# Optimization experiments

Measured on AMD Instinct MI355X. Metric: run time of the kernel, lower is better.

The kernel has to match this reference:

```python
import jax, jax.numpy as jnp
import numpy as np

N_NODES = 100000
N_EDGES = 1600000
D = 128
L = 3
D_OUT = 64


def setup_inputs() -> dict:
    key = jax.random.key(0)
    ks = jax.random.split(key, 6)
    x = jax.random.normal(ks[0], (N_NODES, D), dtype=jnp.float32)
    edge_index = jax.random.randint(ks[1], (2, N_EDGES), 0, N_NODES, dtype=jnp.int64)
    # Kaiming-ish init scale for linear layers
    s = 1.0 / np.sqrt(D)
    W_rel = jax.random.normal(ks[2], (L, D, D), dtype=jnp.float32) * s
    b_rel = jnp.zeros((L, D), dtype=jnp.float32)
    W_root = jax.random.normal(ks[3], (L, D, D), dtype=jnp.float32) * s
    fc_w = jax.random.normal(ks[4], (D_OUT, D), dtype=jnp.float32) * s
    fc_b = jnp.zeros((D_OUT,), dtype=jnp.float32)
    return {"x": x, "edge_index": edge_index, "W_rel": W_rel, "b_rel": b_rel,
            "W_root": W_root, "fc_w": fc_w, "fc_b": fc_b}


def reference(x, edge_index, W_rel, b_rel, W_root, fc_w, fc_b):
    # PyG GraphConv (aggr='add'): x_i' = W_root x_i + W_rel * sum_{j in N(i)} x_j + b
    src, dst = edge_index[0], edge_index[1]
    n = x.shape[0]
    num_layers = W_rel.shape[0]  # static small loop over layers
    for l in range(num_layers):
        agg = jax.ops.segment_sum(x[src], dst, num_segments=n)  # [N, D] scatter-add of gathered neighbor feats
        x = agg @ W_rel[l].T + b_rel[l] + x @ W_root[l].T
    return x @ fc_w.T + fc_b
```

## Files before the change

### kernel.cpp

```cpp
#include <hip/hip_runtime.h>


typedef short bf16x8 __attribute__((ext_vector_type(8)));
typedef float f32x4 __attribute__((ext_vector_type(4)));

#define CAPB 8192

__device__ inline float bf2f(unsigned short u) {
    union { unsigned int i; float f; } v; v.i = ((unsigned int)u) << 16; return v.f;
}
__device__ inline unsigned short f2bf(float f) {
    union { float f; unsigned int i; } v; v.f = f;
    unsigned int r = v.i + 0x7FFFu + ((v.i >> 16) & 1u);
    return (unsigned short)(r >> 16);
}

__global__ __launch_bounds__(256) void stages_kernel(
    const float* __restrict__ Wr0, const float* __restrict__ Wo0,
    const float* __restrict__ Wr1, const float* __restrict__ Wo1,
    const float* __restrict__ Wr2, const float* __restrict__ Wo2,
    const float* __restrict__ fcw, const float* __restrict__ fcb,
    const float* __restrict__ br, unsigned short* __restrict__ Nw,
    float* __restrict__ Bv, int* __restrict__ gcur, int NB) {
    int o = blockIdx.x;
    int t = threadIdx.x;
    __shared__ float c02[128], c12[128], c01[128], c11[128], c21[128];
    __shared__ float redbuf[3][128];

    if (o == 0) {
        for (int q = t; q < NB; q += 256) gcur[q] = 0;
    }

    const float* fo = fcw + (size_t)o * 128;
    int i  = t & 127;
    int hi = t >> 7;

    {
        const float* W = hi ? Wr2 : Wo2;
        float acc = 0.f;
        for (int k = 0; k < 128; k++) acc += W[k * 128 + i] * fo[k];
        (hi ? c12 : c02)[i] = acc;
    }
    __syncthreads();

    if (!hi) {
        float a0 = 0.f, a2 = 0.f;
        for (int k = 0; k < 128; k++) {
            float w1o = Wo1[k * 128 + i], w1r = Wr1[k * 128 + i];
            a0 += w1o * c02[k];
            a2 += w1r * c12[k];
        }
        c01[i] = a0; c21[i] = a2;
    } else {
        float a1 = 0.f;
        for (int k = 0; k < 128; k++)
            a1 += Wr1[k * 128 + i] * c02[k] + Wo1[k * 128 + i] * c12[k];
        c11[i] = a1;
    }
    __syncthreads();

    {
        int p = ((o & 3) << 4) | (o >> 2);
        if (!hi) {
            float a0 = 0.f, a2 = 0.f;
            for (int k = 0; k < 128; k++) {
                float w0 = Wo0[k * 128 + i], wr = Wr0[k * 128 + i];
                a0 += w0 * c01[k];
                a2 += wr * c11[k] + w0 * c21[k];
            }
            Nw[(size_t)p * 512 + 0 * 128 + i] = f2bf(a0);
            Nw[(size_t)p * 512 + 2 * 128 + i] = f2bf(a2);
        } else {
            float a1 = 0.f, a3 = 0.f;
            for (int k = 0; k < 128; k++) {
                float w0 = Wo0[k * 128 + i], wr = Wr0[k * 128 + i];
                a1 += wr * c01[k] + w0 * c11[k];
                a3 += wr * c21[k];
            }
            Nw[(size_t)p * 512 + 1 * 128 + i] = f2bf(a1);
            Nw[(size_t)p * 512 + 3 * 128 + i] = f2bf(a3);
        }
    }

    const float* br0 = br;
    const float* br1 = br + 128;
    const float* br2 = br + 256;
    if (!hi) {
        redbuf[0][i] = br2[i] * fo[i] + br1[i] * c02[i] + br0[i] * c01[i];
        redbuf[1][i] = br1[i] * c12[i] + br0[i] * c11[i];
        redbuf[2][i] = br0[i] * c21[i];
    }
    __syncthreads();
    int w = t >> 6, lane = t & 63;
    if (w < 3) {
        float v = redbuf[w][lane] + redbuf[w][lane + 64];
        for (int off = 32; off; off >>= 1) v += __shfl_down(v, off);
        if (lane == 0) Bv[w * 64 + o] = v + (w == 0 ? fcb[o] : 0.f);
    }
}

__global__ __launch_bounds__(512) void prep_kernel(
    const int* __restrict__ src, const int* __restrict__ dst,
    int* __restrict__ gcur, unsigned int* __restrict__ bucketed, int e, int NA, int NB) {
    int b = blockIdx.x, t = threadIdx.x;
    if (b < NA) {
        __shared__ int sHist[512], sScan[512], sExcl[512], sGbase[512];
        __shared__ unsigned int lbuf[2048];
        __shared__ unsigned short lbkt[2048];
        int e0 = b * 2048;
        int cnt = e - e0; if (cnt > 2048) cnt = 2048;
        sHist[t] = 0;
        __syncthreads();
        unsigned int pk[4]; int bk[4];
#pragma unroll
        for (int k = 0; k < 4; k++) {
            int j = t + k * 512;
            if (j < cnt) {
                int d = dst[e0 + j], s = src[e0 + j];
                bk[k] = d >> 8;
                pk[k] = ((unsigned int)s << 8) | (unsigned int)(d & 255);
                atomicAdd(&sHist[bk[k]], 1);
            } else bk[k] = -1;
        }
        __syncthreads();
        int h = sHist[t];
        if (t < NB && h > 0) sGbase[t] = atomicAdd(&gcur[t], h);
        else sGbase[t] = 0;
        int xv = h; sScan[t] = xv; __syncthreads();
        for (int o = 1; o < 512; o <<= 1) {
            int y = (t >= o) ? sScan[t - o] : 0;
            __syncthreads();
            xv += y; sScan[t] = xv;
            __syncthreads();
        }
        sExcl[t] = xv - h;
        sHist[t] = 0;
        __syncthreads();
#pragma unroll
        for (int k = 0; k < 4; k++) {
            if (bk[k] >= 0) {
                int r = atomicAdd(&sHist[bk[k]], 1);
                int pos = sExcl[bk[k]] + r;
                lbuf[pos] = pk[k];
                lbkt[pos] = (unsigned short)bk[k];
            }
        }
        __syncthreads();
        for (int j = t; j < cnt; j += 512) {
            int b2 = lbkt[j];
            int idx = sGbase[b2] + (j - sExcl[b2]);
            if (idx < CAPB) bucketed[(size_t)b2 * CAPB + idx] = lbuf[j];
        }
    }
}

__global__ __launch_bounds__(256) void partB_kernel(
    const unsigned int* __restrict__ bucketed, const int* __restrict__ gcur,
    int* __restrict__ deg, int* __restrict__ start, int* __restrict__ csr, int n) {
    int b = blockIdx.x, t = threadIdx.x;
    __shared__ int ldeg[256], lscan[256], red[256];
    __shared__ int csr_base_s;
    int cnt = gcur[b]; if (cnt > CAPB) cnt = CAPB;
    int part = 0;
    for (int q = t; q < b; q += 256) { int c = gcur[q]; part += (c > CAPB ? CAPB : c); }
    red[t] = part; __syncthreads();
    for (int o = 128; o > 0; o >>= 1) { if (t < o) red[t] += red[t + o]; __syncthreads(); }
    if (t == 0) csr_base_s = red[0];
    ldeg[t] = 0;
    __syncthreads();
    const unsigned int* bd = bucketed + (size_t)b * CAPB;
    for (int j = t; j < cnt; j += 256) atomicAdd(&ldeg[bd[j] & 255], 1);
    __syncthreads();
    int h = ldeg[t];
    int xv = h; lscan[t] = xv; __syncthreads();
    for (int o = 1; o < 256; o <<= 1) {
        int y = (t >= o) ? lscan[t - o] : 0;
        __syncthreads();
        xv += y; lscan[t] = xv;
        __syncthreads();
    }
    int excl = xv - h;
    int csr_base = csr_base_s;
    int node = b * 256 + t;
    if (node < n) { deg[node] = h; start[node] = csr_base + excl; }
    __syncthreads();
    lscan[t] = excl;
    ldeg[t] = 0;
    __syncthreads();
    for (int j = t; j < cnt; j += 256) {
        unsigned int pkd = bd[j];
        int d = pkd & 255;
        int r = atomicAdd(&ldeg[d], 1);
        csr[csr_base + lscan[d] + r] = (int)(pkd >> 8);
    }
}

__global__ __launch_bounds__(256, 4) void gemm_u_kernel(
    const float* __restrict__ x, const unsigned short* __restrict__ Nw,
    unsigned short* __restrict__ U, int n, int NGB) {
    __shared__ unsigned short Blds[8192];
    int bid   = blockIdx.x;
    int matid = (bid >> 3) & 3;
    int blk   = (bid >> 5) * 8 + (bid & 7);
    if (blk >= NGB) return;
    int tid   = threadIdx.x;

    {
        const uint4* nw4 = (const uint4*)Nw;
        uint4* lds4 = (uint4*)Blds;
        for (int g = tid; g < 1024; g += 256) {
            int slot = g & 63;
            int kq   = g >> 6;
            lds4[g] = nw4[(size_t)slot * 64 + matid * 16 + kq];
        }
    }
    __syncthreads();

    int wave = tid >> 6;
    int lane = tid & 63;
    int m    = lane & 15;
    int quad = lane >> 4;
    size_t n64 = (size_t)n * 64;
    unsigned short* up = U + (size_t)matid * n64;

    const int t0 = blk * 16 + wave * 4;

    float4 v[8];
    {
        int arow = t0 * 16 + m; if (arow >= n) arow = n - 1;
        const float* xr = x + (size_t)arow * 128 + quad * 8;
#pragma unroll
        for (int kk = 0; kk < 4; kk++) {
            v[2 * kk]     = *(const float4*)(xr + kk * 32);
            v[2 * kk + 1] = *(const float4*)(xr + kk * 32 + 4);
        }
    }

#pragma unroll
    for (int it = 0; it < 4; it++) {
        int row0 = (t0 + it) * 16;
        if (row0 >= n) break;

        bf16x8 a[4];
#pragma unroll
        for (int kk = 0; kk < 4; kk++) {
            float4 v0 = v[2 * kk], v1 = v[2 * kk + 1];
            a[kk][0] = (short)f2bf(v0.x); a[kk][1] = (short)f2bf(v0.y);
            a[kk][2] = (short)f2bf(v0.z); a[kk][3] = (short)f2bf(v0.w);
            a[kk][4] = (short)f2bf(v1.x); a[kk][5] = (short)f2bf(v1.y);
            a[kk][6] = (short)f2bf(v1.z); a[kk][7] = (short)f2bf(v1.w);
        }

        if (it < 3) {
            int arow = row0 + 16 + m; if (arow >= n) arow = n - 1;
            const float* xr = x + (size_t)arow * 128 + quad * 8;
#pragma unroll
            for (int kk = 0; kk < 4; kk++) {
                v[2 * kk]     = *(const float4*)(xr + kk * 32);
                v[2 * kk + 1] = *(const float4*)(xr + kk * 32 + 4);
            }
        }

        f32x4 acc[4];
#pragma unroll
        for (int t = 0; t < 4; t++) acc[t] = (f32x4){0.f, 0.f, 0.f, 0.f};
#pragma unroll
        for (int kk = 0; kk < 4; kk++) {
            bf16x8 bq[4];
#pragma unroll
            for (int t = 0; t < 4; t++)
                bq[t] = *(const bf16x8*)(Blds + ((kk * 4 + quad) * 64 + t * 16 + m) * 8);
#pragma unroll
            for (int t = 0; t < 4; t++)
                acc[t] = __builtin_amdgcn_mfma_f32_16x16x32_bf16(a[kk], bq[t], acc[t], 0, 0, 0);
        }

#pragma unroll
        for (int r = 0; r < 4; r++) {
            int orow = row0 + quad * 4 + r;
            if (orow < n) {
                ushort4 o4;
                o4.x = f2bf(acc[0][r]); o4.y = f2bf(acc[1][r]);
                o4.z = f2bf(acc[2][r]); o4.w = f2bf(acc[3][r]);
                *(ushort4*)(up + (size_t)orow * 64 + m * 4) = o4;
            }
        }
    }
}

template <int MODE>
__global__ __launch_bounds__(256) void agg64_kernel(
    const unsigned short* __restrict__ in, const unsigned short* __restrict__ addv,
    const int* __restrict__ csr, const int* __restrict__ start, const int* __restrict__ deg,
    unsigned short* __restrict__ outb, float* __restrict__ outf,
    const float* __restrict__ Bv, int* __restrict__ d2w, const int* __restrict__ d2r, int n) {
    int tid = threadIdx.x;
    int fl  = tid & 7;
    int node = blockIdx.x * 32 + (tid >> 3);
    if (node >= n) return;

    float b0[8], b1[8], b2[8];
    if (MODE == 2) {
#pragma unroll
        for (int j = 0; j < 8; j++) {
            int o = fl * 8 + j;
            b0[j] = Bv[o]; b1[j] = Bv[64 + o]; b2[j] = Bv[128 + o];
        }
    }

    int s0 = start[node];
    int d  = deg[node];

    float acc[8];
#pragma unroll
    for (int j = 0; j < 8; j++) acc[j] = 0.f;
    int dsum = 0;

    int d8 = d & ~7;
    for (int e0 = 0; e0 < d8; e0 += 8) {
        int sv[8];
#pragma unroll
        for (int k = 0; k < 8; k++) sv[k] = csr[s0 + e0 + k];
#pragma unroll
        for (int k = 0; k < 8; k++) {
            bf16x8 v = *(const bf16x8*)(in + (size_t)sv[k] * 64 + fl * 8);
#pragma unroll
            for (int j = 0; j < 8; j++) acc[j] += bf2f((unsigned short)v[j]);
            if (MODE == 0 && fl == 0) dsum += deg[sv[k]];
        }
    }
    for (int i = d8; i < d; i++) {
        int s = csr[s0 + i];
        bf16x8 v = *(const bf16x8*)(in + (size_t)s * 64 + fl * 8);
#pragma unroll
        for (int j = 0; j < 8; j++) acc[j] += bf2f((unsigned short)v[j]);
        if (MODE == 0 && fl == 0) dsum += deg[s];
    }
    if (MODE == 0 && fl == 0) d2w[node] = dsum;

    bf16x8 av = *(const bf16x8*)(addv + (size_t)node * 64 + fl * 8);
    if (MODE < 2) {
        bf16x8 o;
#pragma unroll
        for (int j = 0; j < 8; j++) o[j] = (short)f2bf(acc[j] + bf2f((unsigned short)av[j]));
        *(bf16x8*)(outb + (size_t)node * 64 + fl * 8) = o;
    } else {
        float dg = (float)d;
        float dd = (float)d2r[node];
        float ov[8];
#pragma unroll
        for (int j = 0; j < 8; j++)
            ov[j] = acc[j] + bf2f((unsigned short)av[j]) + b0[j] + dg * b1[j] + dd * b2[j];
        float* op = outf + (size_t)node * 64 + fl * 8;
        *(float4*)(op)     = make_float4(ov[0], ov[1], ov[2], ov[3]);
        *(float4*)(op + 4) = make_float4(ov[4], ov[5], ov[6], ov[7]);
    }
}

extern "C" void kernel_launch(void* const* d_in, const int* in_sizes, int n_in,
                              void* d_out, int out_size, void* d_ws, size_t ws_size,
                              hipStream_t stream) {
    const float* x      = (const float*)d_in[0];
    const int*   ei     = (const int*)d_in[1];
    const float* W_rel  = (const float*)d_in[2];
    const float* b_rel  = (const float*)d_in[3];
    const float* W_root = (const float*)d_in[4];
    const float* fc_w   = (const float*)d_in[5];
    const float* fc_b   = (const float*)d_in[6];

    const int n = in_sizes[0] / 128;
    const int e = in_sizes[1] / 2;
    const int* src = ei;
    const int* dst = ei + e;

    const int NB  = (n + 255) >> 8;
    const int NA  = (e + 2047) / 2048;
    const int NT  = (n + 15) / 16;
    const int NGB = (NT + 15) / 16;
    const int NGBp = (NGB + 7) & ~7;

    char* p = (char*)d_ws;
    auto take = [&](size_t bytes) -> void* {
        void* r = (void*)p;
        p += (bytes + 255) & ~(size_t)255;
        return r;
    };
    unsigned short* U  = (unsigned short*)take((size_t)n * 256 * 2);
    unsigned short* w1 = (unsigned short*)take((size_t)n * 64 * 2);
    unsigned short* w2 = (unsigned short*)take((size_t)n * 64 * 2);
    int* deg    = (int*)take((size_t)n * 4);
    int* start  = (int*)take((size_t)n * 4);
    int* d2     = (int*)take((size_t)n * 4);
    int* csr    = (int*)take((size_t)e * 4);
    unsigned int* bucketed = (unsigned int*)take((size_t)NB * CAPB * 4);
    int* gcur   = (int*)take((size_t)NB * 4);
    unsigned short* Nw = (unsigned short*)take(64 * 512 * 2);
    float* Bv   = (float*)take(192 * 4);

    size_t n64 = (size_t)n * 64;
    unsigned short* u0 = U;
    unsigned short* u1 = U + n64;
    unsigned short* u2 = U + 2 * n64;
    unsigned short* u3 = U + 3 * n64;

    stages_kernel<<<64, 256, 0, stream>>>(
        W_rel, W_root, W_rel + 16384, W_root + 16384,
        W_rel + 2 * 16384, W_root + 2 * 16384,
        fc_w, fc_b, b_rel, Nw, Bv, gcur, NB);
    prep_kernel<<<NA, 512, 0, stream>>>(src, dst, gcur, bucketed, e, NA, NB);
    partB_kernel<<<NB, 256, 0, stream>>>(bucketed, gcur, deg, start, csr, n);

    gemm_u_kernel<<<NGBp * 4, 256, 0, stream>>>(x, Nw, U, n, NGB);

    const int AGB = (n + 31) / 32;
    agg64_kernel<0><<<AGB, 256, 0, stream>>>(
        u3, u2, csr, start, deg, w1, nullptr, nullptr, d2, nullptr, n);
    agg64_kernel<1><<<AGB, 256, 0, stream>>>(
        w1, u1, csr, start, deg, w2, nullptr, nullptr, nullptr, nullptr, n);
    agg64_kernel<2><<<AGB, 256, 0, stream>>>(
        w2, u0, csr, start, deg, nullptr, (float*)d_out, Bv, nullptr, d2, n);
}
```

Measured before the change: 307.6 us.

## Fuse edge bucketing and dense GEMM into one launch via block-range dispatch

Merges the edge-bucketing prep kernel and the x·W GEMM kernel into a single launch whose blocks branch on block index, with shared memory unioned between the two roles. The GEMM does not depend on the bucketing, so the two independent workloads can run concurrently and one launch disappears. The cost is that GEMM blocks now launch with 512 threads and half of them exit after staging the weights, which wastes slots and could lower effective occupancy for the GEMM part.

```diff
diff --git a/kernel.cpp b/kernel.cpp
--- a/kernel.cpp
+++ b/kernel.cpp
@@ -99,17 +99,29 @@
     }
 }
 
-__global__ __launch_bounds__(512) void prep_kernel(
+union FusedSmem {
+    struct {
+        int sHist[512], sScan[512], sExcl[512], sGbase[512];
+        unsigned int lbuf[2048];
+        unsigned short lbkt[2048];
+    } pr;
+    unsigned short Blds[8192];
+};
+
+__global__ __launch_bounds__(512, 4) void fused_kernel(
     const int* __restrict__ src, const int* __restrict__ dst,
-    int* __restrict__ gcur, unsigned int* __restrict__ bucketed, int e, int NA, int NB) {
-    int b = blockIdx.x, t = threadIdx.x;
-    if (b < NA) {
-        __shared__ int sHist[512], sScan[512], sExcl[512], sGbase[512];
-        __shared__ unsigned int lbuf[2048];
-        __shared__ unsigned short lbkt[2048];
+    int* __restrict__ gcur, unsigned int* __restrict__ bucketed, int e, int NA, int NB,
+    const float* __restrict__ x, const unsigned short* __restrict__ Nw,
+    unsigned short* __restrict__ U, int n, int NGB) {
+    __shared__ FusedSmem sm;
+    int bid = blockIdx.x;
+    int t   = threadIdx.x;
+
+    if (bid < NA) {
+        int b = bid;
         int e0 = b * 2048;
         int cnt = e - e0; if (cnt > 2048) cnt = 2048;
-        sHist[t] = 0;
+        sm.pr.sHist[t] = 0;
         __syncthreads();
         unsigned int pk[4]; int bk[4];
 #pragma unroll
@@ -119,37 +131,126 @@
                 int d = dst[e0 + j], s = src[e0 + j];
                 bk[k] = d >> 8;
                 pk[k] = ((unsigned int)s << 8) | (unsigned int)(d & 255);
-                atomicAdd(&sHist[bk[k]], 1);
+                atomicAdd(&sm.pr.sHist[bk[k]], 1);
             } else bk[k] = -1;
         }
         __syncthreads();
-        int h = sHist[t];
-        if (t < NB && h > 0) sGbase[t] = atomicAdd(&gcur[t], h);
-        else sGbase[t] = 0;
-        int xv = h; sScan[t] = xv; __syncthreads();
+        int h = sm.pr.sHist[t];
+        if (t < NB && h > 0) sm.pr.sGbase[t] = atomicAdd(&gcur[t], h);
+        else sm.pr.sGbase[t] = 0;
+        int xv = h; sm.pr.sScan[t] = xv; __syncthreads();
         for (int o = 1; o < 512; o <<= 1) {
-            int y = (t >= o) ? sScan[t - o] : 0;
+            int y = (t >= o) ? sm.pr.sScan[t - o] : 0;
             __syncthreads();
-            xv += y; sScan[t] = xv;
+            xv += y; sm.pr.sScan[t] = xv;
             __syncthreads();
         }
-        sExcl[t] = xv - h;
-        sHist[t] = 0;
+        sm.pr.sExcl[t] = xv - h;
+        sm.pr.sHist[t] = 0;
         __syncthreads();
 #pragma unroll
         for (int k = 0; k < 4; k++) {
             if (bk[k] >= 0) {
-                int r = atomicAdd(&sHist[bk[k]], 1);
-                int pos = sExcl[bk[k]] + r;
-                lbuf[pos] = pk[k];
-                lbkt[pos] = (unsigned short)bk[k];
+                int r = atomicAdd(&sm.pr.sHist[bk[k]], 1);
+                int pos = sm.pr.sExcl[bk[k]] + r;
+                sm.pr.lbuf[pos] = pk[k];
+                sm.pr.lbkt[pos] = (unsigned short)bk[k];
             }
         }
         __syncthreads();
         for (int j = t; j < cnt; j += 512) {
-            int b2 = lbkt[j];
-            int idx = sGbase[b2] + (j - sExcl[b2]);
-            if (idx < CAPB) bucketed[(size_t)b2 * CAPB + idx] = lbuf[j];
+            int b2 = sm.pr.lbkt[j];
+            int idx = sm.pr.sGbase[b2] + (j - sm.pr.sExcl[b2]);
+            if (idx < CAPB) bucketed[(size_t)b2 * CAPB + idx] = sm.pr.lbuf[j];
+        }
+        return;
+    }
+
+    int gbid  = bid - NA;
+    int matid = (gbid >> 3) & 3;
+    int blk   = (gbid >> 5) * 8 + (gbid & 7);
+    if (blk >= NGB) return;
+
+    {
+        const uint4* nw4 = (const uint4*)Nw;
+        uint4* lds4 = (uint4*)sm.Blds;
+        for (int g = t; g < 1024; g += 512) {
+            int slot = g & 63;
+            int kq   = g >> 6;
+            lds4[g] = nw4[(size_t)slot * 64 + matid * 16 + kq];
+        }
+    }
+    __syncthreads();
+    if (t >= 256) return;
+
+    int wave = t >> 6;
+    int lane = t & 63;
+    int m    = lane & 15;
+    int quad = lane >> 4;
+    size_t n64 = (size_t)n * 64;
+    unsigned short* up = U + (size_t)matid * n64;
+
+    const int t0 = blk * 16 + wave * 4;
+
+    float4 v[8];
+    {
+        int arow = t0 * 16 + m; if (arow >= n) arow = n - 1;
+        const float* xr = x + (size_t)arow * 128 + quad * 8;
+#pragma unroll
+        for (int kk = 0; kk < 4; kk++) {
+            v[2 * kk]     = *(const float4*)(xr + kk * 32);
+            v[2 * kk + 1] = *(const float4*)(xr + kk * 32 + 4);
+        }
+    }
+
+#pragma unroll
+    for (int it = 0; it < 4; it++) {
+        int row0 = (t0 + it) * 16;
+        if (row0 >= n) break;
+
+        bf16x8 a[4];
+#pragma unroll
+        for (int kk = 0; kk < 4; kk++) {
+            float4 v0 = v[2 * kk], v1 = v[2 * kk + 1];
+            a[kk][0] = (short)f2bf(v0.x); a[kk][1] = (short)f2bf(v0.y);
+            a[kk][2] = (short)f2bf(v0.z); a[kk][3] = (short)f2bf(v0.w);
+            a[kk][4] = (short)f2bf(v1.x); a[kk][5] = (short)f2bf(v1.y);
+            a[kk][6] = (short)f2bf(v1.z); a[kk][7] = (short)f2bf(v1.w);
+        }
+
+        if (it < 3) {
+            int arow = row0 + 16 + m; if (arow >= n) arow = n - 1;
+            const float* xr = x + (size_t)arow * 128 + quad * 8;
+#pragma unroll
+            for (int kk = 0; kk < 4; kk++) {
+                v[2 * kk]     = *(const float4*)(xr + kk * 32);
+                v[2 * kk + 1] = *(const float4*)(xr + kk * 32 + 4);
+            }
+        }
+
+        f32x4 acc[4];
+#pragma unroll
+        for (int tt = 0; tt < 4; tt++) acc[tt] = (f32x4){0.f, 0.f, 0.f, 0.f};
+#pragma unroll
+        for (int kk = 0; kk < 4; kk++) {
+            bf16x8 bq[4];
+#pragma unroll
+            for (int tt = 0; tt < 4; tt++)
+                bq[tt] = *(const bf16x8*)(sm.Blds + ((kk * 4 + quad) * 64 + tt * 16 + m) * 8);
+#pragma unroll
+            for (int tt = 0; tt < 4; tt++)
+                acc[tt] = __builtin_amdgcn_mfma_f32_16x16x32_bf16(a[kk], bq[tt], acc[tt], 0, 0, 0);
+        }
+
+#pragma unroll
+        for (int r = 0; r < 4; r++) {
+            int orow = row0 + quad * 4 + r;
+            if (orow < n) {
+                ushort4 o4;
+                o4.x = f2bf(acc[0][r]); o4.y = f2bf(acc[1][r]);
+                o4.z = f2bf(acc[2][r]); o4.w = f2bf(acc[3][r]);
+                *(ushort4*)(up + (size_t)orow * 64 + m * 4) = o4;
+            }
         }
     }
 }
@@ -192,99 +293,6 @@
         int d = pkd & 255;
         int r = atomicAdd(&ldeg[d], 1);
         csr[csr_base + lscan[d] + r] = (int)(pkd >> 8);
-    }
-}
-
-__global__ __launch_bounds__(256, 4) void gemm_u_kernel(
-    const float* __restrict__ x, const unsigned short* __restrict__ Nw,
-    unsigned short* __restrict__ U, int n, int NGB) {
-    __shared__ unsigned short Blds[8192];
-    int bid   = blockIdx.x;
-    int matid = (bid >> 3) & 3;
-    int blk   = (bid >> 5) * 8 + (bid & 7);
-    if (blk >= NGB) return;
-    int tid   = threadIdx.x;
-
-    {
-        const uint4* nw4 = (const uint4*)Nw;
-        uint4* lds4 = (uint4*)Blds;
-        for (int g = tid; g < 1024; g += 256) {
-            int slot = g & 63;
-            int kq   = g >> 6;
-            lds4[g] = nw4[(size_t)slot * 64 + matid * 16 + kq];
-        }
-    }
-    __syncthreads();
-
-    int wave = tid >> 6;
-    int lane = tid & 63;
-    int m    = lane & 15;
-    int quad = lane >> 4;
-    size_t n64 = (size_t)n * 64;
-    unsigned short* up = U + (size_t)matid * n64;
-
-    const int t0 = blk * 16 + wave * 4;
-
-    float4 v[8];
-    {
-        int arow = t0 * 16 + m; if (arow >= n) arow = n - 1;
-        const float* xr = x + (size_t)arow * 128 + quad * 8;
-#pragma unroll
-        for (int kk = 0; kk < 4; kk++) {
-            v[2 * kk]     = *(const float4*)(xr + kk * 32);
-            v[2 * kk + 1] = *(const float4*)(xr + kk * 32 + 4);
-        }
-    }
-
-#pragma unroll
-    for (int it = 0; it < 4; it++) {
-        int row0 = (t0 + it) * 16;
-        if (row0 >= n) break;
-
-        bf16x8 a[4];
-#pragma unroll
-        for (int kk = 0; kk < 4; kk++) {
-            float4 v0 = v[2 * kk], v1 = v[2 * kk + 1];
-            a[kk][0] = (short)f2bf(v0.x); a[kk][1] = (short)f2bf(v0.y);
-            a[kk][2] = (short)f2bf(v0.z); a[kk][3] = (short)f2bf(v0.w);
-            a[kk][4] = (short)f2bf(v1.x); a[kk][5] = (short)f2bf(v1.y);
-            a[kk][6] = (short)f2bf(v1.z); a[kk][7] = (short)f2bf(v1.w);
-        }
-
-        if (it < 3) {
-            int arow = row0 + 16 + m; if (arow >= n) arow = n - 1;
-            const float* xr = x + (size_t)arow * 128 + quad * 8;
-#pragma unroll
-            for (int kk = 0; kk < 4; kk++) {
-                v[2 * kk]     = *(const float4*)(xr + kk * 32);
-                v[2 * kk + 1] = *(const float4*)(xr + kk * 32 + 4);
-            }
-        }
-
-        f32x4 acc[4];
-#pragma unroll
-        for (int t = 0; t < 4; t++) acc[t] = (f32x4){0.f, 0.f, 0.f, 0.f};
-#pragma unroll
-        for (int kk = 0; kk < 4; kk++) {
-            bf16x8 bq[4];
-#pragma unroll
-            for (int t = 0; t < 4; t++)
-                bq[t] = *(const bf16x8*)(Blds + ((kk * 4 + quad) * 64 + t * 16 + m) * 8);
-#pragma unroll
-            for (int t = 0; t < 4; t++)
-                acc[t] = __builtin_amdgcn_mfma_f32_16x16x32_bf16(a[kk], bq[t], acc[t], 0, 0, 0);
-        }
-
-#pragma unroll
-        for (int r = 0; r < 4; r++) {
-            int orow = row0 + quad * 4 + r;
-            if (orow < n) {
-                ushort4 o4;
-                o4.x = f2bf(acc[0][r]); o4.y = f2bf(acc[1][r]);
-                o4.z = f2bf(acc[2][r]); o4.w = f2bf(acc[3][r]);
-                *(ushort4*)(up + (size_t)orow * 64 + m * 4) = o4;
-            }
-        }
     }
 }
 
@@ -407,10 +415,11 @@
         W_rel, W_root, W_rel + 16384, W_root + 16384,
         W_rel + 2 * 16384, W_root + 2 * 16384,
         fc_w, fc_b, b_rel, Nw, Bv, gcur, NB);
-    prep_kernel<<<NA, 512, 0, stream>>>(src, dst, gcur, bucketed, e, NA, NB);
+
+    fused_kernel<<<NA + NGBp * 4, 512, 0, stream>>>(
+        src, dst, gcur, bucketed, e, NA, NB, x, Nw, U, n, NGB);
+
     partB_kernel<<<NB, 256, 0, stream>>>(bucketed, gcur, deg, start, csr, n);
-
-    gemm_u_kernel<<<NGBp * 4, 256, 0, stream>>>(x, Nw, U, n, NGB);
 
     const int AGB = (n + 31) / 32;
     agg64_kernel<0><<<AGB, 256, 0, stream>>>(
```

New measurement: 297.5 us. -3.3%, faster.
